# Optimization experiments

Hardware: AMD Instinct MI355X
Metric: run time of the kernel (lower is better)

Reference implementation:

```python
import jax, jax.numpy as jnp
import numpy as np

N_NODES = 50000


def _graph_conv(x, edges, W0, b0, W1, b1):
    # Symmetric (undirected) message passing: each edge (a,b) sends x[b]->a and x[a]->b.
    src = jnp.concatenate([edges[:, 0], edges[:, 1]])  # [2E]
    dst = jnp.concatenate([edges[:, 1], edges[:, 0]])  # [2E]
    deg = jax.ops.segment_sum(jnp.ones_like(dst, dtype=x.dtype), dst, num_segments=N_NODES)
    deg = jnp.maximum(deg, 1.0)  # avoid div-by-zero for isolated nodes
    agg = jax.ops.segment_sum(x[src], dst, num_segments=N_NODES) / deg[:, None]  # [N, F]
    # self transform + normalized-neighbor transform
    return x @ W0 + b0 + agg @ W1 + b1


def setup_inputs() -> dict:
    key = jax.random.key(0)
    ks = jax.random.split(key, 10)
    feats = [256, 512, 256]  # [in] + hidden + [out]
    inp = {
        "vert_features": jax.random.normal(ks[0], (N_NODES, feats[0]), dtype=jnp.float32),
        "edges": jax.random.randint(ks[1], (400000, 2), 0, N_NODES, dtype=jnp.int64),
    }
    kidx = 2
    for l, (fi, fo) in enumerate(zip(feats[:-1], feats[1:])):
        s = 1.0 / np.sqrt(fi)
        inp[f"W0_{l}"] = jax.random.normal(ks[kidx], (fi, fo), dtype=jnp.float32) * s
        inp[f"b0_{l}"] = jnp.zeros((fo,), dtype=jnp.float32)
        inp[f"W1_{l}"] = jax.random.normal(ks[kidx + 1], (fi, fo), dtype=jnp.float32) * s
        inp[f"b1_{l}"] = jnp.zeros((fo,), dtype=jnp.float32)
        kidx += 2
    return inp


def reference(vert_features, edges, W0_0, b0_0, W1_0, b1_0, W0_1, b0_1, W1_1, b1_1):
    # layer 0 + ReLU
    x = _graph_conv(vert_features, edges, W0_0, b0_0, W1_0, b1_0)
    x = jax.nn.relu(x)
    # final layer (no activation)
    x = _graph_conv(x, edges, W0_1, b0_1, W1_1, b1_1)
    return x
```

## Files before the change

kernel.cpp:

```cpp
#include <hip/hip_runtime.h>
#include <stdint.h>

typedef __bf16  bf16x8 __attribute__((ext_vector_type(8)));
typedef float   f32x4  __attribute__((ext_vector_type(4)));
typedef unsigned short u16x8 __attribute__((ext_vector_type(8)));

__device__ __forceinline__ unsigned short f2bf(float f) {
  unsigned int u = __float_as_uint(f);
  u += 0x7fffu + ((u >> 16) & 1u);
  return (unsigned short)(u >> 16);
}
__device__ __forceinline__ float bflo(unsigned int v) { return __uint_as_float(v << 16); }
__device__ __forceinline__ float bfhi(unsigned int v) { return __uint_as_float(v & 0xffff0000u); }

__global__ void detect_fmt_kernel(const int* __restrict__ eg, int* __restrict__ fmt) {
  if (threadIdx.x == 0 && blockIdx.x == 0) {
    int is64 = 1;
    for (int i = 1; i < 32; i += 2) if (eg[i] != 0) { is64 = 0; break; }
    fmt[0] = is64;
  }
}

__global__ void phase1_kernel(const float* __restrict__ x, unsigned short* __restrict__ A0, int n,
                              const int* __restrict__ eg, const int* __restrict__ fmt,
                              int* __restrict__ deg, int E,
                              const float* __restrict__ W00, const float* __restrict__ W10,
                              const float* __restrict__ W01, const float* __restrict__ W11,
                              const float* __restrict__ b00, const float* __restrict__ b10,
                              const float* __restrict__ b01, const float* __restrict__ b11,
                              unsigned short* __restrict__ Bt1, unsigned short* __restrict__ Bt2,
                              float* __restrict__ bias1, float* __restrict__ bias2) {
  const int i = blockIdx.x * 256 + threadIdx.x;
  if (i < n * 64) {
    const int row = i >> 6, c4 = i & 63;
    const float4 v = ((const float4*)x)[i];
    ushort4 o;
    o.x = f2bf(v.x); o.y = f2bf(v.y); o.z = f2bf(v.z); o.w = f2bf(v.w);
    *(ushort4*)&A0[(size_t)row * 512 + c4 * 4] = o;
  }
  if (i < 512 * 512) {
    const int nn = i >> 9, k = i & 511;
    const float v1 = (k < 256) ? W00[k * 512 + nn] : W10[(k - 256) * 512 + nn];
    Bt1[i] = f2bf(v1);
    const float v2 = (nn < 256) ? W01[k * 256 + nn] : W11[k * 256 + (nn - 256)];
    Bt2[i] = f2bf(v2);
    if (i < 512) {
      bias1[i] = b00[i] + b10[i];
      bias2[i] = (i < 256) ? (b01[i] + b11[i]) : 0.f;
    }
  }
  if (i < E) {
    int a, b;
    if (fmt[0]) { a = eg[4 * i]; b = eg[4 * i + 2]; }
    else        { a = eg[2 * i]; b = eg[2 * i + 1]; }
    if ((unsigned)a < (unsigned)n && (unsigned)b < (unsigned)n) {
      atomicAdd(&deg[a], 1);
      atomicAdd(&deg[b], 1);
    }
  }
}

__global__ void block_sum_kernel(const int* __restrict__ deg, int* __restrict__ bsum, int n) {
  const int t = threadIdx.x;
  const int i = blockIdx.x * 1024 + t;
  int v = (i < n) ? deg[i] : 0;
  #pragma unroll
  for (int d = 32; d > 0; d >>= 1) v += __shfl_xor(v, d);
  __shared__ int ws[16];
  if ((t & 63) == 0) ws[t >> 6] = v;
  __syncthreads();
  if (t < 16) {
    int s = ws[t];
    #pragma unroll
    for (int d = 1; d < 16; d <<= 1) s += __shfl_xor(s, d);
    if (t == 0) bsum[blockIdx.x] = s;
  }
}

__global__ void scan_bsum_kernel(int* __restrict__ bsum, int* __restrict__ off, int nb, int n) {
  const int l = threadIdx.x;
  int v = (l < nb) ? bsum[l] : 0;
  const int orig = v;
  #pragma unroll
  for (int d = 1; d < 64; d <<= 1) {
    int u = __shfl_up(v, d);
    if (l >= d) v += u;
  }
  if (l < nb) bsum[l] = v - orig;
  if (l == nb - 1) off[n] = v;
}

__global__ void scan_final_kernel(const int* __restrict__ deg, const int* __restrict__ bsum,
                                  int* __restrict__ off, float* __restrict__ invd,
                                  int* __restrict__ curp, int n) {
  const int t = threadIdx.x;
  const int i = blockIdx.x * 1024 + t;
  const int lane = t & 63, wid = t >> 6;
  const int v = (i < n) ? deg[i] : 0;
  int s = v;
  #pragma unroll
  for (int d = 1; d < 64; d <<= 1) {
    int u = __shfl_up(s, d);
    if (lane >= d) s += u;
  }
  __shared__ int ws[16];
  if (lane == 63) ws[wid] = s;
  __syncthreads();
  if (t < 16) {
    int w = ws[t];
    #pragma unroll
    for (int d = 1; d < 16; d <<= 1) {
      int u = __shfl_up(w, d);
      if (t >= d) w += u;
    }
    ws[t] = w;
  }
  __syncthreads();
  const int add = (wid > 0) ? ws[wid - 1] : 0;
  const int incl = s + add;
  if (i < n) {
    off[i] = bsum[blockIdx.x] + incl - v;
    invd[i] = 1.f / (float)(v > 1 ? v : 1);
    curp[i] = 0;
  }
}

__global__ void fill_kernel(const int* __restrict__ eg, const int* __restrict__ fmt,
                            const int* __restrict__ off, int* __restrict__ cur,
                            int* __restrict__ adj, int E, int n) {
  const int e = blockIdx.x * 256 + threadIdx.x;
  if (e >= E) return;
  int a, b;
  if (fmt[0]) { a = eg[4 * e]; b = eg[4 * e + 2]; }
  else        { a = eg[2 * e]; b = eg[2 * e + 1]; }
  if ((unsigned)a >= (unsigned)n || (unsigned)b >= (unsigned)n) return;
  int p = atomicAdd(&cur[b], 1); adj[off[b] + p] = a;
  int q = atomicAdd(&cur[a], 1); adj[off[a] + q] = b;
}

template<int MODE>
__global__ __launch_bounds__(256) void agg_wide_kernel(
    const unsigned short* __restrict__ T, unsigned short* A0w, float* out,
    const int* __restrict__ adj, const int* __restrict__ off,
    const float* __restrict__ invd, int n) {
  const int node = blockIdx.x * 4 + (threadIdx.x >> 6);
  if (node >= n) return;
  const int lane = threadIdx.x & 63;
  const int half = lane >> 5;
  const int cq = lane & 31;
  constexpr size_t RS = (MODE == 0) ? 512 : 256;
  const int s = off[node], e = off[node + 1];
  float a0 = 0.f, a1 = 0.f, a2 = 0.f, a3 = 0.f, a4 = 0.f, a5 = 0.f, a6 = 0.f, a7 = 0.f;
  for (int base = s; base < e; base += 64) {
    const int cnt = min(64, e - base);
    const int idxv = (lane < cnt) ? adj[base + lane] : 0;
    for (int j = 0; j < cnt; j += 8) {
      uint4 v0 = make_uint4(0u, 0u, 0u, 0u), v1 = v0, v2 = v0, v3 = v0;
      const int s0 = j + 0 + half, s1 = j + 2 + half, s2 = j + 4 + half, s3 = j + 6 + half;
      const int r0 = __shfl(idxv, s0), r1 = __shfl(idxv, s1);
      const int r2 = __shfl(idxv, s2), r3 = __shfl(idxv, s3);
      if (s0 < cnt) v0 = *(const uint4*)&T[(size_t)r0 * RS + cq * 8];
      if (s1 < cnt) v1 = *(const uint4*)&T[(size_t)r1 * RS + cq * 8];
      if (s2 < cnt) v2 = *(const uint4*)&T[(size_t)r2 * RS + cq * 8];
      if (s3 < cnt) v3 = *(const uint4*)&T[(size_t)r3 * RS + cq * 8];
      a0 += bflo(v0.x) + bflo(v1.x) + bflo(v2.x) + bflo(v3.x);
      a1 += bfhi(v0.x) + bfhi(v1.x) + bfhi(v2.x) + bfhi(v3.x);
      a2 += bflo(v0.y) + bflo(v1.y) + bflo(v2.y) + bflo(v3.y);
      a3 += bfhi(v0.y) + bfhi(v1.y) + bfhi(v2.y) + bfhi(v3.y);
      a4 += bflo(v0.z) + bflo(v1.z) + bflo(v2.z) + bflo(v3.z);
      a5 += bfhi(v0.z) + bfhi(v1.z) + bfhi(v2.z) + bfhi(v3.z);
      a6 += bflo(v0.w) + bflo(v1.w) + bflo(v2.w) + bflo(v3.w);
      a7 += bfhi(v0.w) + bfhi(v1.w) + bfhi(v2.w) + bfhi(v3.w);
    }
  }
  a0 += __shfl_xor(a0, 32); a1 += __shfl_xor(a1, 32);
  a2 += __shfl_xor(a2, 32); a3 += __shfl_xor(a3, 32);
  a4 += __shfl_xor(a4, 32); a5 += __shfl_xor(a5, 32);
  a6 += __shfl_xor(a6, 32); a7 += __shfl_xor(a7, 32);
  if (half == 0) {
    const float sc = invd[node];
    if (MODE == 0) {
      u16x8 o;
      o[0] = f2bf(a0 * sc); o[1] = f2bf(a1 * sc); o[2] = f2bf(a2 * sc); o[3] = f2bf(a3 * sc);
      o[4] = f2bf(a4 * sc); o[5] = f2bf(a5 * sc); o[6] = f2bf(a6 * sc); o[7] = f2bf(a7 * sc);
      *(u16x8*)&A0w[(size_t)node * 512 + 256 + cq * 8] = o;
    } else {
      float* po = &out[(size_t)node * 256 + cq * 8];
      float4 p0 = *(float4*)po;
      float4 p1 = *(float4*)(po + 4);
      p0.x += sc * a0; p0.y += sc * a1; p0.z += sc * a2; p0.w += sc * a3;
      p1.x += sc * a4; p1.y += sc * a5; p1.z += sc * a6; p1.w += sc * a7;
      *(float4*)po = p0;
      *(float4*)(po + 4) = p1;
    }
  }
}

template<int MODE>
__global__ __launch_bounds__(256, 4) void gemm_kernel(
    const unsigned short* __restrict__ A, const unsigned short* __restrict__ Bt,
    const float* __restrict__ bias,
    unsigned short* __restrict__ Hout, float* __restrict__ Pout, unsigned short* __restrict__ Zout,
    int M_real, int nwg) {
  constexpr int K = 512;
  constexpr int BK = 32;
  __shared__ unsigned short sm[4][128 * BK];
  const int t = threadIdx.x;
  const int lane = t & 63;
  const int wid = t >> 6;
  const int wr = wid >> 1;
  const int wc = wid & 1;

  const int orig = blockIdx.x;
  const int q = nwg >> 3, r = nwg & 7;
  const int xcd = orig & 7, bidx = orig >> 3;
  const int wgid = (xcd < r ? xcd * (q + 1) : r * (q + 1) + (xcd - r) * q) + bidx;
  const int m0 = (wgid >> 2) * 128;
  const int n0 = (wgid & 3) * 128;

  f32x4 acc[4][4];
  #pragma unroll
  for (int m = 0; m < 4; ++m)
    #pragma unroll
    for (int n = 0; n < 4; ++n)
      acc[m][n] = f32x4{0.f, 0.f, 0.f, 0.f};

  auto stage = [&](int buf, int kt) {
    #pragma unroll
    for (int i = 0; i < 2; ++i) {
      const int row = i * 64 + (t >> 2);
      const int c = (t & 3) ^ ((row >> 1) & 3);
      const unsigned short* ga = A + (size_t)(m0 + row) * K + kt * BK + c * 8;
      __builtin_amdgcn_global_load_lds(
          (const __attribute__((address_space(1))) unsigned int*)ga,
          (__attribute__((address_space(3))) unsigned int*)&sm[buf][(i * 256 + t) * 8], 16, 0, 0);
    }
    #pragma unroll
    for (int i = 0; i < 2; ++i) {
      const int row = i * 64 + (t >> 2);
      const int c = (t & 3) ^ ((row >> 1) & 3);
      const unsigned short* gb = Bt + (size_t)(n0 + row) * K + kt * BK + c * 8;
      __builtin_amdgcn_global_load_lds(
          (const __attribute__((address_space(1))) unsigned int*)gb,
          (__attribute__((address_space(3))) unsigned int*)&sm[2 + buf][(i * 256 + t) * 8], 16, 0, 0);
    }
  };

  auto compute = [&](int buf) {
    bf16x8 aF[4], bF[4];
    #pragma unroll
    for (int m = 0; m < 4; ++m) {
      const int row = wr * 64 + m * 16 + (lane & 15);
      const int sl = (lane >> 4) ^ ((row >> 1) & 3);
      aF[m] = *(const bf16x8*)&sm[buf][row * BK + sl * 8];
    }
    #pragma unroll
    for (int n = 0; n < 4; ++n) {
      const int row = wc * 64 + n * 16 + (lane & 15);
      const int sl = (lane >> 4) ^ ((row >> 1) & 3);
      bF[n] = *(const bf16x8*)&sm[2 + buf][row * BK + sl * 8];
    }
    #pragma unroll
    for (int m = 0; m < 4; ++m)
      #pragma unroll
      for (int n = 0; n < 4; ++n)
        acc[m][n] = __builtin_amdgcn_mfma_f32_16x16x32_bf16(aF[m], bF[n], acc[m][n], 0, 0, 0);
  };

  stage(0, 0);
  __syncthreads();
  int cur = 0;
  #pragma unroll 1
  for (int kt = 0; kt < K / BK - 1; ++kt) {
    stage(cur ^ 1, kt + 1);
    compute(cur);
    __syncthreads();
    cur ^= 1;
  }
  compute(cur);
  __syncthreads();

  if (MODE == 0 || n0 >= 256) {
    unsigned short* ep = &sm[0][0];
    #pragma unroll
    for (int n = 0; n < 4; ++n) {
      const int lcol = wc * 64 + n * 16 + (lane & 15);
      const float bc = (MODE == 0) ? bias[n0 + lcol] : 0.f;
      #pragma unroll
      for (int m = 0; m < 4; ++m) {
        #pragma unroll
        for (int rr = 0; rr < 4; ++rr) {
          const int lr = wr * 64 + m * 16 + (lane >> 4) * 4 + rr;
          float y = acc[m][n][rr] + bc;
          if (MODE == 0) y = y > 0.f ? y : 0.f;
          ep[lr * 128 + (lcol ^ (((lr >> 2) & 7) << 4))] = f2bf(y);
        }
      }
    }
    __syncthreads();
    unsigned short* dst = (MODE == 0) ? Hout : Zout;
    const int ld = (MODE == 0) ? 512 : 256;
    const int cb0 = (MODE == 0) ? n0 : (n0 - 256);
    #pragma unroll
    for (int p = 0; p < 8; ++p) {
      const int tr = p * 16 + (t >> 4);
      const int cb = (t & 15) * 8;
      const uint4 v = *(const uint4*)&ep[tr * 128 + (cb ^ (((tr >> 2) & 7) << 4))];
      *(uint4*)&dst[(size_t)(m0 + tr) * ld + cb0 + cb] = v;
    }
  } else {
    float* ep = (float*)&sm[0][0];
    #pragma unroll
    for (int pp = 0; pp < 2; ++pp) {
      if (wr == pp) {
        #pragma unroll
        for (int n = 0; n < 4; ++n) {
          const int lcol = wc * 64 + n * 16 + (lane & 15);
          const float bc = bias[n0 + lcol];
          #pragma unroll
          for (int m = 0; m < 4; ++m)
            #pragma unroll
            for (int rr = 0; rr < 4; ++rr) {
              const int lr = m * 16 + (lane >> 4) * 4 + rr;
              ep[lr * 128 + (lcol ^ (((lr >> 2) & 7) << 4))] = acc[m][n][rr] + bc;
            }
        }
      }
      __syncthreads();
      const int tr = t >> 2;
      const int grow = m0 + pp * 64 + tr;
      if (grow < M_real) {
        #pragma unroll
        for (int j = 0; j < 8; ++j) {
          const int cb = (t & 3) * 32 + j * 4;
          const float4 v = *(const float4*)&ep[tr * 128 + (cb ^ (((tr >> 2) & 7) << 4))];
          *(float4*)&Pout[(size_t)grow * 256 + n0 + cb] = v;
        }
      }
      __syncthreads();
    }
  }
}

extern "C" void kernel_launch(void* const* d_in, const int* in_sizes, int n_in,
                              void* d_out, int out_size, void* d_ws, size_t ws_size,
                              hipStream_t stream) {
  const float* x   = (const float*)d_in[0];
  const int* edges = (const int*)d_in[1];
  const float* W00 = (const float*)d_in[2];
  const float* b00 = (const float*)d_in[3];
  const float* W10 = (const float*)d_in[4];
  const float* b10 = (const float*)d_in[5];
  const float* W01 = (const float*)d_in[6];
  const float* b01 = (const float*)d_in[7];
  const float* W11 = (const float*)d_in[8];
  const float* b11 = (const float*)d_in[9];
  float* out = (float*)d_out;

  const int n = in_sizes[0] / 256;
  const int E = in_sizes[1] / 2;
  const int Mpad = ((n + 127) / 128) * 128;

  char* p = (char*)d_ws;
  auto alloc = [&](size_t bytes) { char* r = p; p += (bytes + 255) & ~(size_t)255; return r; };
  unsigned short* A0   = (unsigned short*)alloc((size_t)Mpad * 512 * 2);
  unsigned short* H    = (unsigned short*)alloc((size_t)Mpad * 512 * 2);
  unsigned short* Z    = (unsigned short*)alloc((size_t)Mpad * 256 * 2);
  unsigned short* Bt1  = (unsigned short*)alloc(512 * 512 * 2);
  unsigned short* Bt2  = (unsigned short*)alloc(512 * 512 * 2);
  float* bias1 = (float*)alloc(512 * 4);
  float* bias2 = (float*)alloc(512 * 4);
  int*   deg   = (int*)alloc((size_t)n * 4);
  int*   curp  = (int*)alloc((size_t)n * 4);
  int*   off   = (int*)alloc((size_t)(n + 1) * 4);
  int*   bsum  = (int*)alloc(256 * 4);
  float* invd  = (float*)alloc((size_t)n * 4);
  int*   adj   = (int*)alloc((size_t)2 * E * 4);
  int*   fmt   = (int*)alloc(256);

  hipMemsetAsync(deg, 0, (size_t)n * 4, stream);

  detect_fmt_kernel<<<1, 64, 0, stream>>>(edges, fmt);

  const int p1_blocks = (n * 64 + 255) / 256;
  phase1_kernel<<<p1_blocks, 256, 0, stream>>>(x, A0, n, edges, fmt, deg, E,
                                               W00, W10, W01, W11, b00, b10, b01, b11,
                                               Bt1, Bt2, bias1, bias2);

  const int nb = (n + 1023) / 1024;
  block_sum_kernel<<<nb, 1024, 0, stream>>>(deg, bsum, n);
  scan_bsum_kernel<<<1, 64, 0, stream>>>(bsum, off, nb, n);
  scan_final_kernel<<<nb, 1024, 0, stream>>>(deg, bsum, off, invd, curp, n);
  fill_kernel<<<(E + 255) / 256, 256, 0, stream>>>(edges, fmt, off, curp, adj, E, n);

  agg_wide_kernel<0><<<(n + 3) / 4, 256, 0, stream>>>(A0, A0, nullptr, adj, off, invd, n);

  const int nwg = (Mpad / 128) * 4;
  gemm_kernel<0><<<nwg, 256, 0, stream>>>(A0, Bt1, bias1, H, nullptr, nullptr, n, nwg);
  gemm_kernel<1><<<nwg, 256, 0, stream>>>(H, Bt2, bias2, nullptr, out, Z, n, nwg);

  agg_wide_kernel<1><<<(n + 3) / 4, 256, 0, stream>>>(Z, nullptr, out, adj, off, invd, n);
}
```

Baseline: 320.4 us.

## Triple-buffer GEMM K-loop with explicit vmcnt waits and inline edge-format detection

The GEMM main loop moves from double to triple buffering in LDS. It prefetches two k-tiles ahead and uses explicit s_waitcnt vmcnt counts plus raw s_barrier and sched_barrier calls instead of __syncthreads, so global loads overlap more compute. LDS use grows from four to six tiles, and launch bounds drop occupancy from 4 to 3. Separately, the single-thread edge-format detection kernel is removed and each thread checks four words inline, saving one launch but using a weaker heuristic.

Measured after the change: 320.1 us. No clear change (-0.1%).

```diff
diff --git a/kernel.cpp b/kernel.cpp
--- a/kernel.cpp
+++ b/kernel.cpp
@@ -13,17 +13,12 @@
 __device__ __forceinline__ float bflo(unsigned int v) { return __uint_as_float(v << 16); }
 __device__ __forceinline__ float bfhi(unsigned int v) { return __uint_as_float(v & 0xffff0000u); }
 
-__global__ void detect_fmt_kernel(const int* __restrict__ eg, int* __restrict__ fmt) {
-  if (threadIdx.x == 0 && blockIdx.x == 0) {
-    int is64 = 1;
-    for (int i = 1; i < 32; i += 2) if (eg[i] != 0) { is64 = 0; break; }
-    fmt[0] = is64;
-  }
+__device__ __forceinline__ int edges_are_i64(const int* __restrict__ eg) {
+  return (eg[1] | eg[3] | eg[5] | eg[7]) == 0;
 }
 
 __global__ void phase1_kernel(const float* __restrict__ x, unsigned short* __restrict__ A0, int n,
-                              const int* __restrict__ eg, const int* __restrict__ fmt,
-                              int* __restrict__ deg, int E,
+                              const int* __restrict__ eg, int* __restrict__ deg, int E,
                               const float* __restrict__ W00, const float* __restrict__ W10,
                               const float* __restrict__ W01, const float* __restrict__ W11,
                               const float* __restrict__ b00, const float* __restrict__ b10,
@@ -51,8 +46,8 @@
   }
   if (i < E) {
     int a, b;
-    if (fmt[0]) { a = eg[4 * i]; b = eg[4 * i + 2]; }
-    else        { a = eg[2 * i]; b = eg[2 * i + 1]; }
+    if (edges_are_i64(eg)) { a = eg[4 * i]; b = eg[4 * i + 2]; }
+    else                   { a = eg[2 * i]; b = eg[2 * i + 1]; }
     if ((unsigned)a < (unsigned)n && (unsigned)b < (unsigned)n) {
       atomicAdd(&deg[a], 1);
       atomicAdd(&deg[b], 1);
@@ -125,14 +120,14 @@
   }
 }
 
-__global__ void fill_kernel(const int* __restrict__ eg, const int* __restrict__ fmt,
+__global__ void fill_kernel(const int* __restrict__ eg,
                             const int* __restrict__ off, int* __restrict__ cur,
                             int* __restrict__ adj, int E, int n) {
   const int e = blockIdx.x * 256 + threadIdx.x;
   if (e >= E) return;
   int a, b;
-  if (fmt[0]) { a = eg[4 * e]; b = eg[4 * e + 2]; }
-  else        { a = eg[2 * e]; b = eg[2 * e + 1]; }
+  if (edges_are_i64(eg)) { a = eg[4 * e]; b = eg[4 * e + 2]; }
+  else                   { a = eg[2 * e]; b = eg[2 * e + 1]; }
   if ((unsigned)a >= (unsigned)n || (unsigned)b >= (unsigned)n) return;
   int p = atomicAdd(&cur[b], 1); adj[off[b] + p] = a;
   int q = atomicAdd(&cur[a], 1); adj[off[a] + q] = b;
@@ -197,14 +192,15 @@
 }
 
 template<int MODE>
-__global__ __launch_bounds__(256, 4) void gemm_kernel(
+__global__ __launch_bounds__(256, 3) void gemm_kernel(
     const unsigned short* __restrict__ A, const unsigned short* __restrict__ Bt,
     const float* __restrict__ bias,
     unsigned short* __restrict__ Hout, float* __restrict__ Pout, unsigned short* __restrict__ Zout,
     int M_real, int nwg) {
   constexpr int K = 512;
   constexpr int BK = 32;
-  __shared__ unsigned short sm[4][128 * BK];
+  constexpr int NT = K / BK;
+  __shared__ unsigned short sm[6][128 * BK];
   const int t = threadIdx.x;
   const int lane = t & 63;
   const int wid = t >> 6;
@@ -242,8 +238,10 @@
       const unsigned short* gb = Bt + (size_t)(n0 + row) * K + kt * BK + c * 8;
       __builtin_amdgcn_global_load_lds(
           (const __attribute__((address_space(1))) unsigned int*)gb,
-          (__attribute__((address_space(3))) unsigned int*)&sm[2 + buf][(i * 256 + t) * 8], 16, 0, 0);
-    }
+          (__attribute__((address_space(3))) unsigned int*)&sm[3 + buf][(i * 256 + t) * 8], 16, 0, 0);
+    }
+    asm volatile("" ::: "memory");
+    __builtin_amdgcn_sched_barrier(0);
   };
 
   auto compute = [&](int buf) {
@@ -258,7 +256,7 @@
     for (int n = 0; n < 4; ++n) {
       const int row = wc * 64 + n * 16 + (lane & 15);
       const int sl = (lane >> 4) ^ ((row >> 1) & 3);
-      bF[n] = *(const bf16x8*)&sm[2 + buf][row * BK + sl * 8];
+      bF[n] = *(const bf16x8*)&sm[3 + buf][row * BK + sl * 8];
     }
     #pragma unroll
     for (int m = 0; m < 4; ++m)
@@ -268,16 +266,22 @@
   };
 
   stage(0, 0);
-  __syncthreads();
-  int cur = 0;
+  stage(1, 1);
   #pragma unroll 1
-  for (int kt = 0; kt < K / BK - 1; ++kt) {
-    stage(cur ^ 1, kt + 1);
-    compute(cur);
-    __syncthreads();
-    cur ^= 1;
-  }
-  compute(cur);
+  for (int kt = 0; kt < NT; ++kt) {
+    if (kt + 2 < NT) stage((kt + 2) % 3, kt + 2);
+    if (kt < NT - 2)       { asm volatile("s_waitcnt vmcnt(8)" ::: "memory"); }
+    else if (kt == NT - 2) { asm volatile("s_waitcnt vmcnt(4)" ::: "memory"); }
+    else                   { asm volatile("s_waitcnt vmcnt(0)" ::: "memory"); }
+    __builtin_amdgcn_sched_barrier(0);
+    __builtin_amdgcn_s_barrier();
+    __builtin_amdgcn_sched_barrier(0);
+    compute(kt % 3);
+    asm volatile("s_waitcnt lgkmcnt(0)" ::: "memory");
+    __builtin_amdgcn_sched_barrier(0);
+    __builtin_amdgcn_s_barrier();
+    __builtin_amdgcn_sched_barrier(0);
+  }
   __syncthreads();
 
   if (MODE == 0 || n0 >= 256) {
@@ -376,14 +380,11 @@
   int*   bsum  = (int*)alloc(256 * 4);
   float* invd  = (float*)alloc((size_t)n * 4);
   int*   adj   = (int*)alloc((size_t)2 * E * 4);
-  int*   fmt   = (int*)alloc(256);
 
   hipMemsetAsync(deg, 0, (size_t)n * 4, stream);
 
-  detect_fmt_kernel<<<1, 64, 0, stream>>>(edges, fmt);
-
   const int p1_blocks = (n * 64 + 255) / 256;
-  phase1_kernel<<<p1_blocks, 256, 0, stream>>>(x, A0, n, edges, fmt, deg, E,
+  phase1_kernel<<<p1_blocks, 256, 0, stream>>>(x, A0, n, edges, deg, E,
                                                W00, W10, W01, W11, b00, b10, b01, b11,
                                                Bt1, Bt2, bias1, bias2);
 
@@ -391,7 +392,7 @@
   block_sum_kernel<<<nb, 1024, 0, stream>>>(deg, bsum, n);
   scan_bsum_kernel<<<1, 64, 0, stream>>>(bsum, off, nb, n);
   scan_final_kernel<<<nb, 1024, 0, stream>>>(deg, bsum, off, invd, curp, n);
-  fill_kernel<<<(E + 255) / 256, 256, 0, stream>>>(edges, fmt, off, curp, adj, E, n);
+  fill_kernel<<<(E + 255) / 256, 256, 0, stream>>>(edges, off, curp, adj, E, n);
 
   agg_wide_kernel<0><<<(n + 3) / 4, 256, 0, stream>>>(A0, A0, nullptr, adj, off, invd, n);
 
```
